# Performance work log

Hardware: AMD Instinct MI355X
Metric: run time of the kernel (lower is better)

The kernel has to match this reference:

```python
import math
import jax, jax.numpy as jnp
import numpy as np

_EPS = 1e-8

def _nan_to_num(x):
    return jnp.where(jnp.isfinite(x), x, jnp.zeros((), x.dtype))

def _norm(x, axis=-1, keepdims=False):
    return jnp.sqrt(jnp.sum(x * x, axis=axis, keepdims=keepdims) + _EPS)

def _normalize(x, axis=-1):
    return _nan_to_num(x / _norm(x, axis=axis, keepdims=True))

def _dihedrals(X, eps=1e-7):
    # X: [B, N, A, 3]; use first 3 backbone atoms, flatten to [B, 3N, 3]
    B, N = X.shape[0], X.shape[1]
    Xf = X[:, :, :3].reshape(B, 3 * N, 3)
    dX = Xf[:, 1:] - Xf[:, :-1]
    U = _normalize(dX)
    u_2, u_1, u_0 = U[:, :-2], U[:, 1:-1], U[:, 2:]
    n_2 = _normalize(jnp.cross(u_2, u_1))
    n_1 = _normalize(jnp.cross(u_1, u_0))
    cosD = jnp.clip(jnp.sum(n_2 * n_1, -1), -1 + eps, 1 - eps)
    D = jnp.sign(jnp.sum(u_2 * n_1, -1)) * jnp.arccos(cosD)
    D = jnp.pad(D, ((0, 0), (1, 2)))
    D = D.reshape(B, N, 3)
    return jnp.concatenate([jnp.cos(D), jnp.sin(D)], axis=-1)  # [B, N, 6]

def _orientations(X):
    # X: [B, N, 3] (CA coords)
    fwd = _normalize(X[:, 1:] - X[:, :-1])
    bwd = _normalize(X[:, :-1] - X[:, 1:])
    fwd = jnp.pad(fwd, ((0, 0), (0, 1), (0, 0)))
    bwd = jnp.pad(bwd, ((0, 0), (1, 0), (0, 0)))
    return jnp.concatenate([fwd[:, :, None], bwd[:, :, None]], axis=-2)  # [B, N, 2, 3]

def _sidechains(X):
    n, origin, c = X[:, :, 0], X[:, :, 1], X[:, :, 2]
    c = _normalize(c - origin)
    n = _normalize(n - origin)
    bisector = _normalize(c + n)
    perp = _normalize(jnp.cross(c, n))
    return -bisector * math.sqrt(1.0 / 3.0) - perp * math.sqrt(2.0 / 3.0)  # [B, N, 3]

def _dist(X, coord_mask, res_idx, padding_mask, top_k, order=3):
    # X: [B, N, 3] CA coords
    B, N = X.shape[0], X.shape[1]
    cm2 = coord_mask[:, None, :] & coord_mask[:, :, None]        # [B, N, N]
    rm = ~padding_mask
    rm2 = rm[:, None, :] & rm[:, :, None]
    dX = X[:, None, :, :] - X[:, :, None, :]                     # [B, N, N, 3]
    D = cm2 * _norm(dX)                                          # masked pairwise dists
    cov = (jnp.abs(res_idx[..., None] - res_idx[..., None, :]) <= order).astype(D.dtype)
    D_cov = D * (1.0 - cov)
    seq = jnp.arange(N)
    Dseq = jnp.abs(seq[None, :] - seq[:, None]).astype(D.dtype)[None]  # [1, N, N]
    D_adjust = _nan_to_num(D_cov) + (~cm2) * (1e8 + Dseq * 1e6) + (~rm2) * 1e10
    k = min(int(top_k), N)
    # smallest-k via top_k on negated distances
    _, E_idx = jax.lax.top_k(-D_adjust, k)                       # [B, N, k]
    D_neighbors = jnp.take_along_axis(D, E_idx, axis=-1)
    coord_mask_neighbors = D_neighbors < 5e7
    residue_mask_neighbors = D_neighbors < 5e9
    return D_neighbors, E_idx, coord_mask_neighbors, residue_mask_neighbors


def setup_inputs() -> dict:
    key = jax.random.key(0)
    k1, k2 = jax.random.split(key)
    B, N = 8, 2048
    coords = jax.random.normal(k1, (B, N, 3, 3), dtype=jnp.float32) * 10.0
    coord_mask = jax.random.bernoulli(k2, 0.9, (B, N))
    res_idx = jnp.broadcast_to(jnp.arange(N, dtype=jnp.int32), (B, N))
    padding_mask = jnp.zeros((B, N), dtype=bool)
    return {"coords": coords, "coord_mask": coord_mask, "res_idx": res_idx,
            "padding_mask": padding_mask, "top_k": 30}


def reference(coords, coord_mask, res_idx, padding_mask, top_k):
    node_scalar = jnp.concatenate(
        [_dihedrals(coords), coord_mask.astype(jnp.float32)[..., None]], axis=-1)  # [B, N, 7]
    X_ca = coords[:, :, 1]
    orient = _orientations(X_ca)            # [B, N, 2, 3]
    side = _sidechains(coords)              # [B, N, 3]
    node_vector = jnp.concatenate([orient, side[:, :, None]], axis=-2)  # [B, N, 3, 3]
    D_neighbors, E_idx, cm_nb, rm_nb = _dist(X_ca, coord_mask, res_idx, padding_mask, top_k)
    return node_scalar, node_vector, D_neighbors, E_idx, cm_nb, rm_nb
```

## Files before the change

kernel.cpp:

```cpp
#include <hip/hip_runtime.h>

#define BB 8
#define NN 2048
#define KK 30
#define UNKV  0xFFFFFFFEu
#define EMPV  0xFFFFFFFFu
#define SENTJ 0xFFFFFFFFu

__device__ __forceinline__ float norm3_eps_exact(float dx, float dy, float dz) {
    float s = __fadd_rn(__fadd_rn(__fmul_rn(dx, dx), __fmul_rn(dy, dy)), __fmul_rn(dz, dz));
    return __fsqrt_rn(__fadd_rn(s, 1e-8f));
}

__device__ __forceinline__ void normalize3f(float x, float y, float z, float* o) {
    float s = x * x + y * y + z * z + 1e-8f;
    float inv = __builtin_amdgcn_rsqf(s);
    o[0] = x * inv; o[1] = y * inv; o[2] = z * inv;
}

template <int CTRL>
__device__ __forceinline__ unsigned dppmin(unsigned v) {
    unsigned t = (unsigned)__builtin_amdgcn_update_dpp((int)v, (int)v, CTRL, 0xF, 0xF, false);
    return (t < v) ? t : v;
}
__device__ __forceinline__ unsigned wave_min_last(unsigned v) {
    v = dppmin<0xB1>(v);
    v = dppmin<0x4E>(v);
    v = dppmin<0x141>(v);
    v = dppmin<0x140>(v);
    v = dppmin<0x142>(v);
    v = dppmin<0x143>(v);
    return v;
}

__device__ __forceinline__ unsigned key_bits(const float4* __restrict__ Pb, int i, unsigned j,
                                             float xi, float yi, float zi, bool cmi_on) {
    int dd = i - (int)j;
    unsigned dj = (dd < 0) ? (unsigned)(-dd) : (unsigned)dd;
    float penB = __fadd_rn(1e8f, __fmul_rn((float)dj, 1e6f));
    float adj;
    if (cmi_on) {
        float4 p = Pb[j];
        bool cmj = ((int)__float_as_uint(p.w)) < 0;
        float nrm = norm3_eps_exact(p.x - xi, p.y - yi, p.z - zi);
        adj = cmj ? ((dj <= 3u) ? 0.0f : nrm) : penB;
    } else {
        adj = penB;
    }
    return __float_as_uint(adj);
}

__global__ __launch_bounds__(256) void prep_kernel(const float* __restrict__ coords,
                                                   const int* __restrict__ cmask,
                                                   float* __restrict__ out_scalar,
                                                   float* __restrict__ out_vec,
                                                   float4* __restrict__ P) {
    __shared__ float sm[258 * 9];
    int b  = blockIdx.x >> 3;
    int n0 = (blockIdx.x & 7) << 8;
    int tid = threadIdx.x;
    const float* gbase = coords + (size_t)b * NN * 9;
    int lof = (n0 - 1) * 9;
    for (int idx = tid; idx < 258 * 9; idx += 256) {
        int gidx = lof + idx;
        sm[idx] = ((unsigned)gidx < (unsigned)(NN * 9)) ? gbase[gidx] : 0.0f;
    }
    __syncthreads();

    const float* lbase = sm - lof;
    int n  = n0 + tid;
    int bn = b * NN + n;

    float cosv[3], sinv[3];
    #pragma unroll
    for (int t = 0; t < 3; ++t) {
        int m = 3 * n + t;
        if (m < 1 || m > 3 * NN - 3) { cosv[t] = 1.0f; sinv[t] = 0.0f; continue; }
        const float* p0 = lbase + (m - 1) * 3;
        const float* p1 = lbase + (m    ) * 3;
        const float* p2 = lbase + (m + 1) * 3;
        const float* p3 = lbase + (m + 2) * 3;
        float u2[3], u1[3], u0[3];
        normalize3f(p1[0]-p0[0], p1[1]-p0[1], p1[2]-p0[2], u2);
        normalize3f(p2[0]-p1[0], p2[1]-p1[1], p2[2]-p1[2], u1);
        normalize3f(p3[0]-p2[0], p3[1]-p2[1], p3[2]-p2[2], u0);
        float c21[3] = { u2[1]*u1[2]-u2[2]*u1[1], u2[2]*u1[0]-u2[0]*u1[2], u2[0]*u1[1]-u2[1]*u1[0] };
        float c10[3] = { u1[1]*u0[2]-u1[2]*u0[1], u1[2]*u0[0]-u1[0]*u0[2], u1[0]*u0[1]-u1[1]*u0[0] };
        float n2[3], n1v[3];
        normalize3f(c21[0], c21[1], c21[2], n2);
        normalize3f(c10[0], c10[1], c10[2], n1v);
        float cd = n2[0]*n1v[0] + n2[1]*n1v[1] + n2[2]*n1v[2];
        cd = fminf(fmaxf(cd, -1.0f + 1e-7f), 1.0f - 1e-7f);
        float sg = u2[0]*n1v[0] + u2[1]*n1v[1] + u2[2]*n1v[2];
        float sgn = (sg > 0.0f) ? 1.0f : ((sg < 0.0f) ? -1.0f : 0.0f);
        cosv[t] = (sgn == 0.0f) ? 1.0f : cd;
        sinv[t] = sgn * sqrtf(fmaxf(0.0f, 1.0f - cd * cd));
    }
    int cm = cmask[bn];
    float* os = out_scalar + (size_t)bn * 7;
    os[0] = cosv[0]; os[1] = cosv[1]; os[2] = cosv[2];
    os[3] = sinv[0]; os[4] = sinv[1]; os[5] = sinv[2];
    os[6] = cm ? 1.0f : 0.0f;

    const float* ca = lbase + (n * 3 + 1) * 3;
    float cx = ca[0], cy = ca[1], cz = ca[2];
    P[(size_t)b * NN + n] = make_float4(cx, cy, cz, __uint_as_float(cm ? 0x80000000u : 0u));

    float fwd[3] = {0.f, 0.f, 0.f}, bwd[3] = {0.f, 0.f, 0.f};
    if (n < NN - 1) {
        const float* cn = lbase + ((n + 1) * 3 + 1) * 3;
        normalize3f(cn[0]-cx, cn[1]-cy, cn[2]-cz, fwd);
    }
    if (n > 0) {
        const float* cp = lbase + ((n - 1) * 3 + 1) * 3;
        normalize3f(cp[0]-cx, cp[1]-cy, cp[2]-cz, bwd);
    }
    const float* pn = lbase + (n * 3 + 0) * 3;
    const float* pc = lbase + (n * 3 + 2) * 3;
    float cv[3], nv[3];
    normalize3f(pc[0]-cx, pc[1]-cy, pc[2]-cz, cv);
    normalize3f(pn[0]-cx, pn[1]-cy, pn[2]-cz, nv);
    float bis[3];
    normalize3f(cv[0]+nv[0], cv[1]+nv[1], cv[2]+nv[2], bis);
    float cr[3] = { cv[1]*nv[2]-cv[2]*nv[1], cv[2]*nv[0]-cv[0]*nv[2], cv[0]*nv[1]-cv[1]*nv[0] };
    float perp[3];
    normalize3f(cr[0], cr[1], cr[2], perp);
    const float s13 = 0.57735026918962576f;
    const float s23 = 0.81649658092772603f;
    float* ov = out_vec + (size_t)bn * 9;
    ov[0] = fwd[0]; ov[1] = fwd[1]; ov[2] = fwd[2];
    ov[3] = bwd[0]; ov[4] = bwd[1]; ov[5] = bwd[2];
    ov[6] = -bis[0]*s13 - perp[0]*s23;
    ov[7] = -bis[1]*s13 - perp[1]*s23;
    ov[8] = -bis[2]*s13 - perp[2]*s23;
}

__global__ __launch_bounds__(256, 8) void knn_kernel(
        const float4* __restrict__ P,
        const int* __restrict__ cmask,
        float* __restrict__ outD, float* __restrict__ outE,
        float* __restrict__ outC, float* __restrict__ outR) {
    unsigned lane = threadIdx.x & 63u;
    int wv  = threadIdx.x >> 6;
    int row = __builtin_amdgcn_readfirstlane(blockIdx.x * 4 + wv);
    int b = row >> 11, i = row & (NN - 1);

    const float4* Pb = P + (size_t)b * NN;
    bool cmi = (__builtin_amdgcn_readfirstlane(cmask[row]) != 0);

    float4 pi = Pb[i];
    float xi = pi.x, yi = pi.y, zi = pi.z;

    unsigned v1[4], j1[4], v2[4], j2[4];
    #pragma unroll
    for (int g = 0; g < 4; ++g) { v1[g] = EMPV; j1[g] = SENTJ; v2[g] = EMPV; j2[g] = SENTJ; }

    #pragma unroll
    for (int g = 0; g < 4; ++g) {
        #pragma unroll
        for (int t = 0; t < 8; ++t) {
            unsigned j = lane + 64u * (unsigned)(8 * g + t);
            unsigned kb = key_bits(Pb, i, j, xi, yi, zi, cmi);
            bool lt1 = kb < v1[g], lt2 = kb < v2[g];
            v2[g] = lt1 ? v1[g] : (lt2 ? kb : v2[g]);
            j2[g] = lt1 ? j1[g] : (lt2 ? j  : j2[g]);
            v1[g] = lt1 ? kb : v1[g];
            j1[g] = lt1 ? j  : j1[g];
        }
    }

    unsigned consumed = 0, winj = 0, lval, lj;
    lval = v1[0]; lj = j1[0];
    #pragma unroll
    for (int g = 1; g < 4; ++g) { if (v1[g] < lval) { lval = v1[g]; lj = j1[g]; } }

    #pragma unroll 1
    for (int r = 0; r < KK; ++r) {
        unsigned mv = wave_min_last(lval);
        unsigned s_v = (unsigned)__builtin_amdgcn_readlane((int)mv, 63);
        unsigned cj = (lval == s_v) ? lj : SENTJ;
        unsigned mj = wave_min_last(cj);
        unsigned s_j = (unsigned)__builtin_amdgcn_readlane((int)mj, 63);

        winj = (lane == (unsigned)r) ? s_j : winj;

        #pragma unroll
        for (int g = 0; g < 4; ++g) {
            bool match = (j1[g] == s_j);
            v1[g] = match ? v2[g] : v1[g];
            j1[g] = match ? j2[g] : j1[g];
            v2[g] = match ? UNKV : v2[g];
        }
        unsigned slot = s_j >> 6;
        bool own = (lane == (s_j & 63u));
        consumed = own ? (consumed | (1u << slot)) : consumed;

        bool need = (v1[0] == UNKV) | (v1[1] == UNKV) | (v1[2] == UNKV) | (v1[3] == UNKV);
        if (__any(need)) {
            #pragma unroll
            for (int g = 0; g < 4; ++g) {
                if (v1[g] == UNKV) {
                    unsigned nv1 = EMPV, nj1 = SENTJ, nv2 = EMPV, nj2 = SENTJ;
                    #pragma unroll 1
                    for (int t = 0; t < 8; ++t) {
                        unsigned jj = lane + 64u * (unsigned)(8 * g + t);
                        unsigned kb = ((consumed >> (unsigned)(8 * g + t)) & 1u)
                                        ? EMPV : key_bits(Pb, i, jj, xi, yi, zi, cmi);
                        bool lt1 = kb < nv1, lt2 = kb < nv2;
                        nv2 = lt1 ? nv1 : (lt2 ? kb : nv2);
                        nj2 = lt1 ? nj1 : (lt2 ? jj : nj2);
                        nv1 = lt1 ? kb : nv1;
                        nj1 = lt1 ? jj : nj1;
                    }
                    v1[g] = nv1; j1[g] = nj1; v2[g] = nv2; j2[g] = nj2;
                }
            }
        }
        lval = v1[0]; lj = j1[0];
        #pragma unroll
        for (int g = 1; g < 4; ++g) { if (v1[g] < lval) { lval = v1[g]; lj = j1[g]; } }
    }

    if (lane < KK) {
        unsigned j = winj;
        float4 p = Pb[j];
        bool cmj = ((int)__float_as_uint(p.w)) < 0;
        float nrm = norm3_eps_exact(p.x - xi, p.y - yi, p.z - zi);
        float D = (cmi && cmj) ? nrm : 0.0f;
        int o = row * KK + (int)lane;
        outD[o] = D;
        outE[o] = (float)j;
        outC[o] = (D < 5.0e7f) ? 1.0f : 0.0f;
        outR[o] = (D < 5.0e9f) ? 1.0f : 0.0f;
    }
}

extern "C" void kernel_launch(void* const* d_in, const int* in_sizes, int n_in,
                              void* d_out, int out_size, void* d_ws, size_t ws_size,
                              hipStream_t stream) {
    const float* coords = (const float*)d_in[0];
    const int*   cmask  = (const int*)d_in[1];

    float* out = (float*)d_out;
    float* out_scalar = out;
    float* out_vec    = out_scalar + (size_t)BB * NN * 7;
    float* outD       = out_vec    + (size_t)BB * NN * 9;
    float* outE       = outD       + (size_t)BB * NN * KK;
    float* outC       = outE       + (size_t)BB * NN * KK;
    float* outR       = outC       + (size_t)BB * NN * KK;

    float4* P = (float4*)d_ws;

    hipLaunchKernelGGL(prep_kernel, dim3(BB * 8), dim3(256), 0, stream,
                       coords, cmask, out_scalar, out_vec, P);
    hipLaunchKernelGGL(knn_kernel, dim3(BB * NN / 4), dim3(256), 0, stream,
                       P, cmask, outD, outE, outC, outR);
}
```

Baseline: 155.9 us.

## Process two query rows per wavefront with half-wave reductions and ballot fast path

Each 64-lane wavefront now handles two rows, one per 32-lane half, with each lane scanning 64 candidates in 8 groups instead of 32 in 4. The per-round reduction drops one DPP step, and a ballot-based fast path skips the second index reduction when the minimum is unique in each half. Refills are limited to the groups that held the winners. This halves the number of wavefronts and shortens the serial reduction chain, at the cost of more registers per lane and a longer initial scan per lane.

```diff
diff --git a/kernel.cpp b/kernel.cpp
--- a/kernel.cpp
+++ b/kernel.cpp
@@ -6,6 +6,7 @@
 #define UNKV  0xFFFFFFFEu
 #define EMPV  0xFFFFFFFFu
 #define SENTJ 0xFFFFFFFFu
+typedef unsigned long long ull;
 
 __device__ __forceinline__ float norm3_eps_exact(float dx, float dy, float dz) {
     float s = __fadd_rn(__fadd_rn(__fmul_rn(dx, dx), __fmul_rn(dy, dy)), __fmul_rn(dz, dz));
@@ -23,30 +24,24 @@
     unsigned t = (unsigned)__builtin_amdgcn_update_dpp((int)v, (int)v, CTRL, 0xF, 0xF, false);
     return (t < v) ? t : v;
 }
-__device__ __forceinline__ unsigned wave_min_last(unsigned v) {
+__device__ __forceinline__ unsigned half_min32(unsigned v) {
     v = dppmin<0xB1>(v);
     v = dppmin<0x4E>(v);
     v = dppmin<0x141>(v);
     v = dppmin<0x140>(v);
     v = dppmin<0x142>(v);
-    v = dppmin<0x143>(v);
     return v;
 }
 
-__device__ __forceinline__ unsigned key_bits(const float4* __restrict__ Pb, int i, unsigned j,
-                                             float xi, float yi, float zi, bool cmi_on) {
+__device__ __forceinline__ unsigned key_of(float4 p, int i, unsigned j,
+                                           float xi, float yi, float zi, bool cmi) {
     int dd = i - (int)j;
     unsigned dj = (dd < 0) ? (unsigned)(-dd) : (unsigned)dd;
     float penB = __fadd_rn(1e8f, __fmul_rn((float)dj, 1e6f));
-    float adj;
-    if (cmi_on) {
-        float4 p = Pb[j];
-        bool cmj = ((int)__float_as_uint(p.w)) < 0;
-        float nrm = norm3_eps_exact(p.x - xi, p.y - yi, p.z - zi);
-        adj = cmj ? ((dj <= 3u) ? 0.0f : nrm) : penB;
-    } else {
-        adj = penB;
-    }
+    float nrm = norm3_eps_exact(p.x - xi, p.y - yi, p.z - zi);
+    float a   = (dj <= 3u) ? 0.0f : nrm;
+    bool cmj  = ((int)__float_as_uint(p.w)) < 0;
+    float adj = (cmi && cmj) ? a : penB;
     return __float_as_uint(adj);
 }
 
@@ -141,93 +136,116 @@
         float* __restrict__ outD, float* __restrict__ outE,
         float* __restrict__ outC, float* __restrict__ outR) {
     unsigned lane = threadIdx.x & 63u;
+    unsigned l5   = lane & 31u;
+    bool     hh   = lane >= 32u;
     int wv  = threadIdx.x >> 6;
-    int row = __builtin_amdgcn_readfirstlane(blockIdx.x * 4 + wv);
-    int b = row >> 11, i = row & (NN - 1);
+    int row = blockIdx.x * 8 + wv * 2 + (hh ? 1 : 0);
+    int b   = blockIdx.x >> 8;
+    int i   = row & (NN - 1);
 
     const float4* Pb = P + (size_t)b * NN;
-    bool cmi = (__builtin_amdgcn_readfirstlane(cmask[row]) != 0);
+    bool cmi = (cmask[row] != 0);
 
     float4 pi = Pb[i];
     float xi = pi.x, yi = pi.y, zi = pi.z;
 
-    unsigned v1[4], j1[4], v2[4], j2[4];
+    unsigned v1[8], j1[8], v2[8], j2[8];
+
     #pragma unroll
-    for (int g = 0; g < 4; ++g) { v1[g] = EMPV; j1[g] = SENTJ; v2[g] = EMPV; j2[g] = SENTJ; }
-
-    #pragma unroll
-    for (int g = 0; g < 4; ++g) {
+    for (int g = 0; g < 8; ++g) {
+        unsigned nv1 = EMPV, nj1 = SENTJ, nv2 = EMPV, nj2 = SENTJ;
         #pragma unroll
-        for (int t = 0; t < 8; ++t) {
-            unsigned j = lane + 64u * (unsigned)(8 * g + t);
-            unsigned kb = key_bits(Pb, i, j, xi, yi, zi, cmi);
-            bool lt1 = kb < v1[g], lt2 = kb < v2[g];
-            v2[g] = lt1 ? v1[g] : (lt2 ? kb : v2[g]);
-            j2[g] = lt1 ? j1[g] : (lt2 ? j  : j2[g]);
-            v1[g] = lt1 ? kb : v1[g];
-            j1[g] = lt1 ? j  : j1[g];
-        }
-    }
-
-    unsigned consumed = 0, winj = 0, lval, lj;
+        for (int s = 0; s < 8; ++s) {
+            unsigned j = l5 + 32u * (unsigned)(8 * g + s);
+            unsigned kb = key_of(Pb[j], i, j, xi, yi, zi, cmi);
+            bool lt1 = kb < nv1, lt2 = kb < nv2;
+            nv2 = lt1 ? nv1 : (lt2 ? kb : nv2);
+            nj2 = lt1 ? nj1 : (lt2 ? j  : nj2);
+            nv1 = lt1 ? kb : nv1;
+            nj1 = lt1 ? j  : nj1;
+        }
+        v1[g] = nv1; j1[g] = nj1; v2[g] = nv2; j2[g] = nj2;
+    }
+
+    ull consumed = 0ull;
+    unsigned winj = 0u, lval, lj;
     lval = v1[0]; lj = j1[0];
     #pragma unroll
-    for (int g = 1; g < 4; ++g) { if (v1[g] < lval) { lval = v1[g]; lj = j1[g]; } }
+    for (int g = 1; g < 8; ++g) { if (v1[g] < lval) { lval = v1[g]; lj = j1[g]; } }
 
     #pragma unroll 1
     for (int r = 0; r < KK; ++r) {
-        unsigned mv = wave_min_last(lval);
-        unsigned s_v = (unsigned)__builtin_amdgcn_readlane((int)mv, 63);
-        unsigned cj = (lval == s_v) ? lj : SENTJ;
-        unsigned mj = wave_min_last(cj);
-        unsigned s_j = (unsigned)__builtin_amdgcn_readlane((int)mj, 63);
-
-        winj = (lane == (unsigned)r) ? s_j : winj;
-
+        unsigned mv  = half_min32(lval);
+        unsigned sv0 = (unsigned)__builtin_amdgcn_readlane((int)mv, 31);
+        unsigned sv1 = (unsigned)__builtin_amdgcn_readlane((int)mv, 63);
+        unsigned svv = hh ? sv1 : sv0;
+        bool tie = (lval == svv);
+        ull bal = __ballot(tie);
+        unsigned m0 = (unsigned)bal, m1 = (unsigned)(bal >> 32);
+        unsigned sj0, sj1;
+        if (__popc(m0) == 1 && __popc(m1) == 1) {
+            sj0 = (unsigned)__builtin_amdgcn_readlane((int)lj, __builtin_ctz(m0));
+            sj1 = (unsigned)__builtin_amdgcn_readlane((int)lj, 32 + __builtin_ctz(m1));
+        } else {
+            unsigned cj = tie ? lj : SENTJ;
+            unsigned mj = half_min32(cj);
+            sj0 = (unsigned)__builtin_amdgcn_readlane((int)mj, 31);
+            sj1 = (unsigned)__builtin_amdgcn_readlane((int)mj, 63);
+        }
+        unsigned sjv = hh ? sj1 : sj0;
+        winj = (l5 == (unsigned)r) ? winj * 0u + sjv : winj;
+
+        unsigned g0 = sj0 >> 8, g1 = sj1 >> 8;
+        bool need = false;
         #pragma unroll
-        for (int g = 0; g < 4; ++g) {
-            bool match = (j1[g] == s_j);
-            v1[g] = match ? v2[g] : v1[g];
-            j1[g] = match ? j2[g] : j1[g];
-            v2[g] = match ? UNKV : v2[g];
-        }
-        unsigned slot = s_j >> 6;
-        bool own = (lane == (s_j & 63u));
-        consumed = own ? (consumed | (1u << slot)) : consumed;
-
-        bool need = (v1[0] == UNKV) | (v1[1] == UNKV) | (v1[2] == UNKV) | (v1[3] == UNKV);
+        for (int g = 0; g < 8; ++g) {
+            if ((unsigned)g == g0 || (unsigned)g == g1) {
+                bool match = (j1[g] == sjv);
+                v1[g] = match ? v2[g] : v1[g];
+                j1[g] = match ? j2[g] : j1[g];
+                v2[g] = match ? UNKV  : v2[g];
+                need = need | (v1[g] == UNKV);
+            }
+        }
+        bool own = (l5 == (sjv & 31u));
+        unsigned tb = sjv >> 5;
+        consumed |= own ? (1ull << tb) : 0ull;
+
         if (__any(need)) {
             #pragma unroll
-            for (int g = 0; g < 4; ++g) {
-                if (v1[g] == UNKV) {
-                    unsigned nv1 = EMPV, nj1 = SENTJ, nv2 = EMPV, nj2 = SENTJ;
-                    #pragma unroll 1
-                    for (int t = 0; t < 8; ++t) {
-                        unsigned jj = lane + 64u * (unsigned)(8 * g + t);
-                        unsigned kb = ((consumed >> (unsigned)(8 * g + t)) & 1u)
-                                        ? EMPV : key_bits(Pb, i, jj, xi, yi, zi, cmi);
-                        bool lt1 = kb < nv1, lt2 = kb < nv2;
-                        nv2 = lt1 ? nv1 : (lt2 ? kb : nv2);
-                        nj2 = lt1 ? nj1 : (lt2 ? jj : nj2);
-                        nv1 = lt1 ? kb : nv1;
-                        nj1 = lt1 ? jj : nj1;
+            for (int g = 0; g < 8; ++g) {
+                if ((unsigned)g == g0 || (unsigned)g == g1) {
+                    if (v1[g] == UNKV) {
+                        unsigned nv1 = EMPV, nj1 = SENTJ, nv2 = EMPV, nj2 = SENTJ;
+                        #pragma unroll
+                        for (int s = 0; s < 8; ++s) {
+                            int t = 8 * g + s;
+                            unsigned j = l5 + 32u * (unsigned)t;
+                            unsigned kb = key_of(Pb[j], i, j, xi, yi, zi, cmi);
+                            kb = ((unsigned)(consumed >> t) & 1u) ? EMPV : kb;
+                            bool lt1 = kb < nv1, lt2 = kb < nv2;
+                            nv2 = lt1 ? nv1 : (lt2 ? kb : nv2);
+                            nj2 = lt1 ? nj1 : (lt2 ? j  : nj2);
+                            nv1 = lt1 ? kb : nv1;
+                            nj1 = lt1 ? j  : nj1;
+                        }
+                        v1[g] = nv1; j1[g] = nj1; v2[g] = nv2; j2[g] = nj2;
                     }
-                    v1[g] = nv1; j1[g] = nj1; v2[g] = nv2; j2[g] = nj2;
                 }
             }
         }
         lval = v1[0]; lj = j1[0];
         #pragma unroll
-        for (int g = 1; g < 4; ++g) { if (v1[g] < lval) { lval = v1[g]; lj = j1[g]; } }
-    }
-
-    if (lane < KK) {
+        for (int g = 1; g < 8; ++g) { if (v1[g] < lval) { lval = v1[g]; lj = j1[g]; } }
+    }
+
+    if (l5 < KK) {
         unsigned j = winj;
         float4 p = Pb[j];
         bool cmj = ((int)__float_as_uint(p.w)) < 0;
         float nrm = norm3_eps_exact(p.x - xi, p.y - yi, p.z - zi);
         float D = (cmi && cmj) ? nrm : 0.0f;
-        int o = row * KK + (int)lane;
+        int o = row * KK + (int)l5;
         outD[o] = D;
         outE[o] = (float)j;
         outC[o] = (D < 5.0e7f) ? 1.0f : 0.0f;
@@ -253,6 +271,6 @@
 
     hipLaunchKernelGGL(prep_kernel, dim3(BB * 8), dim3(256), 0, stream,
                        coords, cmask, out_scalar, out_vec, P);
-    hipLaunchKernelGGL(knn_kernel, dim3(BB * NN / 4), dim3(256), 0, stream,
+    hipLaunchKernelGGL(knn_kernel, dim3(BB * NN / 8), dim3(256), 0, stream,
                        P, cmask, outD, outE, outC, outR);
 }
```

Result: slower. 395.9 us (+154.0%).
